# Kernel optimization log

Measured on AMD Instinct MI355X. Metric: run time of the kernel, lower is better.

Reference implementation:

```python
import jax, jax.numpy as jnp
import numpy as np
import math

NUM_BUCKETS = 32
MAX_DISTANCE = 128
N_HEADS = 16
D_KV = 64


def _relative_position_bucket(relative_position, num_buckets=NUM_BUCKETS, max_distance=MAX_DISTANCE):
    # bidirectional (encoder) variant
    num_buckets //= 2
    relative_buckets = (relative_position > 0).astype(jnp.int32) * num_buckets
    rp = jnp.abs(relative_position)
    max_exact = num_buckets // 2
    is_small = rp < max_exact
    rp_large = max_exact + (
        jnp.log(jnp.maximum(rp, 1).astype(jnp.float32) / max_exact)
        / math.log(max_distance / max_exact)
        * (num_buckets - max_exact)
    ).astype(jnp.int32)
    rp_large = jnp.minimum(rp_large, num_buckets - 1)
    return relative_buckets + jnp.where(is_small, rp, rp_large)


def compute_bias(rel_bias, q_len, k_len):
    ctx = jnp.arange(q_len)[:, None]
    mem = jnp.arange(k_len)[None, :]
    buckets = _relative_position_bucket(mem - ctx)          # [q, k]
    values = rel_bias[buckets]                               # [q, k, h]
    return jnp.transpose(values, (2, 0, 1))[None]            # [1, h, q, k]


def setup_inputs() -> dict:
    key = jax.random.key(0)
    ks = jax.random.split(key, 6)
    d_model, inner = 1024, N_HEADS * D_KV
    s = 0.02
    return {
        "hidden_states": jax.random.normal(ks[0], (2, 2048, d_model), jnp.float32),
        "Wq": jax.random.normal(ks[1], (d_model, inner), jnp.float32) * s,
        "Wk": jax.random.normal(ks[2], (d_model, inner), jnp.float32) * s,
        "Wv": jax.random.normal(ks[3], (d_model, inner), jnp.float32) * s,
        "Wo": jax.random.normal(ks[4], (inner, d_model), jnp.float32) * s,
        "rel_bias": jax.random.normal(ks[5], (NUM_BUCKETS, N_HEADS), jnp.float32) * s,
    }


def reference(hidden_states, Wq, Wk, Wv, Wo, rel_bias):
    B, S, D = hidden_states.shape

    def split_heads(x):  # [B,S,inner] -> [B,H,S,dk]
        return x.reshape(B, S, N_HEADS, D_KV).transpose(0, 2, 1, 3)

    q = split_heads(hidden_states @ Wq)
    k = split_heads(hidden_states @ Wk)
    v = split_heads(hidden_states @ Wv)

    # T5 does NOT scale by 1/sqrt(d_kv)
    scores = jnp.einsum("bhqd,bhkd->bhqk", q, k)
    scores = scores + compute_bias(rel_bias, S, S)
    attn = jax.nn.softmax(scores, axis=-1)
    ctx = jnp.einsum("bhqk,bhkd->bhqd", attn, v)
    ctx = ctx.transpose(0, 2, 1, 3).reshape(B, S, N_HEADS * D_KV)
    return ctx @ Wo
```

## Files before the change

### kernel.cpp

```cpp
#include <hip/hip_runtime.h>
#include <hip/hip_bf16.h>

typedef __bf16 bf16x8 __attribute__((ext_vector_type(8)));
typedef __bf16 bf16x4 __attribute__((ext_vector_type(4)));
typedef float floatx4 __attribute__((ext_vector_type(4)));
using bf16 = __hip_bfloat16;

#define S_    2048
#define NHEAD 16
#define LOG2E 1.4426950408889634f

__device__ __forceinline__ void load_lds16(const bf16* g, void* lds) {
  __builtin_amdgcn_global_load_lds((const __attribute__((address_space(1))) void*)g,
                                   (__attribute__((address_space(3))) void*)lds, 16, 0, 0);
}

__global__ void prep_kernel(const float* __restrict__ hidden,
                            const float* __restrict__ wq, const float* __restrict__ wk,
                            const float* __restrict__ wv, const float* __restrict__ wo,
                            const float* __restrict__ rel_bias,
                            bf16* __restrict__ hbf, bf16* __restrict__ wt_qkv,
                            bf16* __restrict__ wt_o, float* __restrict__ tab) {
  __shared__ bf16 tile[32][33];
  int bid = blockIdx.x;
  if (bid < 4096) {
    int i = (bid * 256 + threadIdx.x) * 4;
    float4 v = *(const float4*)(hidden + i);
    bf16 o[4] = {__float2bfloat16(v.x), __float2bfloat16(v.y),
                 __float2bfloat16(v.z), __float2bfloat16(v.w)};
    *(uint2*)(hbf + i) = *(const uint2*)o;
  } else if (bid < 8192) {
    int r = bid - 4096;
    int mat = r >> 10;
    int rem = r & 1023;
    int n0 = (rem & 31) * 32, k0 = (rem >> 5) * 32;
    int tx = threadIdx.x & 31, ty = threadIdx.x >> 5;
    const float* src = (mat == 0) ? wq : (mat == 1) ? wk : (mat == 2) ? wv : wo;
    bf16* dst = (mat == 3) ? wt_o : wt_qkv + mat * 1024 * 1024;
#pragma unroll
    for (int j = 0; j < 32; j += 8)
      tile[ty + j][tx] = __float2bfloat16(src[(k0 + ty + j) * 1024 + n0 + tx]);
    __syncthreads();
#pragma unroll
    for (int j = 0; j < 32; j += 8)
      dst[(n0 + ty + j) * 1024 + k0 + tx] = tile[tx][ty + j];
  } else {
    int idx = (bid - 8192) * 256 + threadIdx.x;
    int h = idx >> 12, j = idx & 4095;
    int delta = j - 2048;
    int rb = (delta > 0) ? 16 : 0;
    int rpa = delta < 0 ? -delta : delta;
    int bsmall;
    if (rpa < 8) {
      bsmall = rpa;
    } else {
      int lg = 25 - __clz(rpa * rpa);
      bsmall = 8 + lg;
      if (bsmall > 15) bsmall = 15;
    }
    tab[idx] = rel_bias[(rb + bsmall) * 16 + h] * LOG2E;
  }
}

__global__ __launch_bounds__(256) void gemm_qkv_kernel(const bf16* __restrict__ A,
                                                       const bf16* __restrict__ Bt,
                                                       bf16* __restrict__ qh,
                                                       bf16* __restrict__ kf,
                                                       bf16* __restrict__ vf) {
  const int K = 1024;
  __shared__ bf16 As[128 * 32];
  __shared__ bf16 Bs[128 * 32];
  int t = threadIdx.x;
  int m0 = blockIdx.y * 128, n0 = blockIdx.x * 128;
  int w = t >> 6, lane = t & 63, ln = lane & 15, quad = lane >> 4;
  int wr = w >> 1, wc = w & 1;
  floatx4 acc[4][4];
  floatx4 zero = {0.f, 0.f, 0.f, 0.f};
#pragma unroll
  for (int i = 0; i < 4; i++)
#pragma unroll
    for (int j = 0; j < 4; j++) acc[i][j] = zero;

  int r = t >> 2, c = (t & 3) * 8;
  const bf16* Ag = A + (long)(m0 + r) * K + c;
  const bf16* Bg = Bt + (long)(n0 + r) * K + c;
  char* ldsA0 = (char*)As + w * 1024;
  char* ldsA1 = ldsA0 + 4096;
  char* ldsB0 = (char*)Bs + w * 1024;
  char* ldsB1 = ldsB0 + 4096;

  for (int k0 = 0; k0 < K; k0 += 32) {
    load_lds16(Ag + k0, ldsA0);
    load_lds16(Ag + (long)64 * K + k0, ldsA1);
    load_lds16(Bg + k0, ldsB0);
    load_lds16(Bg + (long)64 * K + k0, ldsB1);
    __syncthreads();
    bf16x8 af[4], bfv[4];
#pragma unroll
    for (int i = 0; i < 4; i++)
      af[i] = *(const bf16x8*)&As[(wr * 64 + i * 16 + ln) * 32 + quad * 8];
#pragma unroll
    for (int j = 0; j < 4; j++)
      bfv[j] = *(const bf16x8*)&Bs[(wc * 64 + j * 16 + ln) * 32 + quad * 8];
#pragma unroll
    for (int i = 0; i < 4; i++)
#pragma unroll
      for (int j = 0; j < 4; j++)
        acc[i][j] = __builtin_amdgcn_mfma_f32_16x16x32_bf16(af[i], bfv[j], acc[i][j], 0, 0, 0);
    __syncthreads();
  }

  int nb = n0 + wc * 64;
  int type = nb >> 10, h = (nb >> 6) & 15;
  int b = (m0 >> 11);
  int sl0 = (m0 & 2047) + wr * 64;
  long bhbase = (long)((b * 16 + h)) * 131072;

  if (type == 0) {
#pragma unroll
    for (int i = 0; i < 4; i++)
#pragma unroll
      for (int j = 0; j < 4; j++) {
        int d = j * 16 + ln;
#pragma unroll
        for (int rr = 0; rr < 4; rr++) {
          int s = sl0 + i * 16 + quad * 4 + rr;
          qh[bhbase + (long)s * 64 + d] = __float2bfloat16(acc[i][j][rr]);
        }
      }
  } else if (type == 1) {
#pragma unroll
    for (int i = 0; i < 4; i++)
#pragma unroll
      for (int j = 0; j < 4; j++) {
        int d = j * 16 + ln;
        int dpart = (d >> 5) * 512 + ((d >> 3) & 3) * 128 + (d & 7);
        int kb = (sl0 + i * 16) * 64;
#pragma unroll
        for (int rr = 0; rr < 4; rr++)
          kf[bhbase + kb + dpart + (quad * 4 + rr) * 8] = __float2bfloat16(acc[i][j][rr]);
      }
  } else {
#pragma unroll
    for (int i = 0; i < 4; i++)
#pragma unroll
      for (int j = 0; j < 4; j++) {
        int off = (sl0 + (i >> 1) * 32) * 64 + j * 512 +
                  ((quad >> 1) + ((i & 1) << 1)) * 128 + ln * 8 + (quad & 1) * 4;
        bf16x4 pk = {(__bf16)acc[i][j][0], (__bf16)acc[i][j][1],
                     (__bf16)acc[i][j][2], (__bf16)acc[i][j][3]};
        *(bf16x4*)(vf + bhbase + off) = pk;
      }
  }
}

__global__ __launch_bounds__(256, 2) void attn_kernel(const bf16* __restrict__ qh,
                                                      const bf16* __restrict__ kf,
                                                      const bf16* __restrict__ vf,
                                                      const float* __restrict__ btab,
                                                      bf16* __restrict__ ctx) {
  __shared__ char PsRaw[4 * 2048];
  __shared__ char KV[2][16384];
  int t = threadIdx.x, w = t >> 6, lane = t & 63, ln = lane & 15, quad = lane >> 4;
  int bh = blockIdx.x, b = bh >> 4, h = bh & 15;
  int qw = blockIdx.y * 64 + w * 16;

  const bf16* qbase = qh + (long)bh * S_ * 64;
  const bf16* kfb = kf + (long)bh * S_ * 64;
  const bf16* vfb = vf + (long)bh * S_ * 64;
  const float* bt = btab + h * 4096;
  char* myPs = PsRaw + w * 2048;
  int lbo = quad * 256 + ln * 16;

  bf16x8 Qf0, Qf1;
  {
    const bf16* qr = qbase + (long)(qw + ln) * 64;
    Qf0 = *(const bf16x8*)(qr + quad * 8);
    Qf1 = *(const bf16x8*)(qr + 32 + quad * 8);
  }

  float cneg = bt[0], cpos = bt[4095];
  float l_acc = 0.f;
  floatx4 o[4];
  floatx4 zero = {0.f, 0.f, 0.f, 0.f};
#pragma unroll
  for (int dt = 0; dt < 4; dt++) o[dt] = zero;

  {
    const bf16* kg = kfb + t * 8;
    const bf16* vg = vfb + t * 8;
    load_lds16(kg,        KV[0] + w * 1024);
    load_lds16(kg + 2048, KV[0] + 4096 + w * 1024);
    load_lds16(vg,        KV[0] + 8192 + w * 1024);
    load_lds16(vg + 2048, KV[0] + 12288 + w * 1024);
  }

  int pb = 0;
  for (int k0 = 0; k0 < S_; k0 += 64) {
    __syncthreads();
    int kn = k0 + 64;
    if (kn < S_) {
      const bf16* kg = kfb + (long)kn * 64 + t * 8;
      const bf16* vg = vfb + (long)kn * 64 + t * 8;
      char* nb_ = KV[pb ^ 1];
      load_lds16(kg,        nb_ + w * 1024);
      load_lds16(kg + 2048, nb_ + 4096 + w * 1024);
      load_lds16(vg,        nb_ + 8192 + w * 1024);
      load_lds16(vg + 2048, nb_ + 12288 + w * 1024);
    }

    const char* bK = KV[pb];
    const char* bV = KV[pb] + 8192;
    bf16x8 Kr[4][2], Vr[4][2];
#pragma unroll
    for (int tile = 0; tile < 4; tile++) {
      Kr[tile][0] = *(const bf16x8*)(bK + tile * 2048 + lbo);
      Kr[tile][1] = *(const bf16x8*)(bK + tile * 2048 + 1024 + lbo);
    }
#pragma unroll
    for (int f = 0; f < 2; f++)
#pragma unroll
      for (int dt = 0; dt < 4; dt++)
        Vr[dt][f] = *(const bf16x8*)(bV + f * 4096 + dt * 1024 + lbo);

    bool near = (k0 > qw - 192) && (k0 < qw + 144);
    float bl[16];
    if (near) {
      int bb = k0 + quad * 4 - (qw + ln) + 2048;
#pragma unroll
      for (int tile = 0; tile < 4; tile++)
#pragma unroll
        for (int rr = 0; rr < 4; rr++)
          bl[tile * 4 + rr] = bt[bb + tile * 16 + rr];
    }

    floatx4 st[4];
#pragma unroll
    for (int tile = 0; tile < 4; tile++) {
      st[tile] = __builtin_amdgcn_mfma_f32_16x16x32_bf16(Kr[tile][0], Qf0, zero, 0, 0, 0);
      st[tile] = __builtin_amdgcn_mfma_f32_16x16x32_bf16(Kr[tile][1], Qf1, st[tile], 0, 0, 0);
    }

    if (near) {
#pragma unroll
      for (int tile = 0; tile < 4; tile++) {
        float p0 = __builtin_amdgcn_exp2f(fmaf(st[tile][0], LOG2E, bl[tile * 4 + 0]));
        float p1 = __builtin_amdgcn_exp2f(fmaf(st[tile][1], LOG2E, bl[tile * 4 + 1]));
        float p2 = __builtin_amdgcn_exp2f(fmaf(st[tile][2], LOG2E, bl[tile * 4 + 2]));
        float p3 = __builtin_amdgcn_exp2f(fmaf(st[tile][3], LOG2E, bl[tile * 4 + 3]));
        l_acc += (p0 + p1) + (p2 + p3);
        bf16x4 pk = {(__bf16)p0, (__bf16)p1, (__bf16)p2, (__bf16)p3};
        int chunk = tile * 2 + (quad >> 1);
        *(bf16x4*)(myPs + (ln * 8 + (chunk ^ (ln & 7))) * 16 + (quad & 1) * 8) = pk;
      }
    } else {
      float cb = (k0 > qw) ? cpos : cneg;
#pragma unroll
      for (int tile = 0; tile < 4; tile++) {
        float p0 = __builtin_amdgcn_exp2f(fmaf(st[tile][0], LOG2E, cb));
        float p1 = __builtin_amdgcn_exp2f(fmaf(st[tile][1], LOG2E, cb));
        float p2 = __builtin_amdgcn_exp2f(fmaf(st[tile][2], LOG2E, cb));
        float p3 = __builtin_amdgcn_exp2f(fmaf(st[tile][3], LOG2E, cb));
        l_acc += (p0 + p1) + (p2 + p3);
        bf16x4 pk = {(__bf16)p0, (__bf16)p1, (__bf16)p2, (__bf16)p3};
        int chunk = tile * 2 + (quad >> 1);
        *(bf16x4*)(myPs + (ln * 8 + (chunk ^ (ln & 7))) * 16 + (quad & 1) * 8) = pk;
      }
    }

    bf16x8 Pf0 = *(const bf16x8*)(myPs + (ln * 8 + (quad ^ (ln & 7))) * 16);
    bf16x8 Pf1 = *(const bf16x8*)(myPs + (ln * 8 + ((4 + quad) ^ (ln & 7))) * 16);
#pragma unroll
    for (int dt = 0; dt < 4; dt++) {
      o[dt] = __builtin_amdgcn_mfma_f32_16x16x32_bf16(Pf0, Vr[dt][0], o[dt], 0, 0, 0);
      o[dt] = __builtin_amdgcn_mfma_f32_16x16x32_bf16(Pf1, Vr[dt][1], o[dt], 0, 0, 0);
    }

    pb ^= 1;
  }

  l_acc += __shfl_xor(l_acc, 16);
  l_acc += __shfl_xor(l_acc, 32);
#pragma unroll
  for (int rr = 0; rr < 4; rr++) {
    float linv = 1.0f / __shfl(l_acc, quad * 4 + rr);
    int q = qw + quad * 4 + rr;
#pragma unroll
    for (int dt = 0; dt < 4; dt++)
      ctx[(long)(b * S_ + q) * 1024 + h * 64 + dt * 16 + ln] =
          __float2bfloat16(o[dt][rr] * linv);
  }
}

__global__ __launch_bounds__(256) void gemm_bt_kernel(const bf16* __restrict__ A,
                                                      const bf16* __restrict__ Bt,
                                                      float* __restrict__ C,
                                                      int M, int N, int K) {
  __shared__ bf16 As[128 * 32];
  __shared__ bf16 Bs[128 * 32];
  int t = threadIdx.x;
  int m0 = blockIdx.y * 128, n0 = blockIdx.x * 128;
  int w = t >> 6, lane = t & 63, ln = lane & 15, quad = lane >> 4;
  int wr = w >> 1, wc = w & 1;
  floatx4 acc[4][4];
  floatx4 zero = {0.f, 0.f, 0.f, 0.f};
#pragma unroll
  for (int i = 0; i < 4; i++)
#pragma unroll
    for (int j = 0; j < 4; j++) acc[i][j] = zero;

  int r = t >> 2, c = (t & 3) * 8;
  const bf16* Ag = A + (long)(m0 + r) * K + c;
  const bf16* Bg = Bt + (long)(n0 + r) * K + c;
  char* ldsA0 = (char*)As + w * 1024;
  char* ldsA1 = ldsA0 + 4096;
  char* ldsB0 = (char*)Bs + w * 1024;
  char* ldsB1 = ldsB0 + 4096;

  for (int k0 = 0; k0 < K; k0 += 32) {
    load_lds16(Ag + k0, ldsA0);
    load_lds16(Ag + (long)64 * K + k0, ldsA1);
    load_lds16(Bg + k0, ldsB0);
    load_lds16(Bg + (long)64 * K + k0, ldsB1);
    __syncthreads();
    bf16x8 af[4], bfv[4];
#pragma unroll
    for (int i = 0; i < 4; i++)
      af[i] = *(const bf16x8*)&As[(wr * 64 + i * 16 + ln) * 32 + quad * 8];
#pragma unroll
    for (int j = 0; j < 4; j++)
      bfv[j] = *(const bf16x8*)&Bs[(wc * 64 + j * 16 + ln) * 32 + quad * 8];
#pragma unroll
    for (int i = 0; i < 4; i++)
#pragma unroll
      for (int j = 0; j < 4; j++)
        acc[i][j] = __builtin_amdgcn_mfma_f32_16x16x32_bf16(af[i], bfv[j], acc[i][j], 0, 0, 0);
    __syncthreads();
  }

#pragma unroll
  for (int i = 0; i < 4; i++)
#pragma unroll
    for (int j = 0; j < 4; j++)
#pragma unroll
      for (int rr = 0; rr < 4; rr++)
        C[(long)(m0 + wr * 64 + i * 16 + quad * 4 + rr) * N + n0 + wc * 64 + j * 16 + ln] =
            acc[i][j][rr];
}

extern "C" void kernel_launch(void* const* d_in, const int* in_sizes, int n_in,
                              void* d_out, int out_size, void* d_ws, size_t ws_size,
                              hipStream_t stream) {
  (void)in_sizes; (void)n_in; (void)out_size; (void)ws_size;
  const float* hidden   = (const float*)d_in[0];
  const float* Wq       = (const float*)d_in[1];
  const float* Wk       = (const float*)d_in[2];
  const float* Wv       = (const float*)d_in[3];
  const float* Wo       = (const float*)d_in[4];
  const float* rel_bias = (const float*)d_in[5];

  char* ws = (char*)d_ws;
  bf16*  hbf    = (bf16*)(ws + 0);
  bf16*  wt_qkv = (bf16*)(ws + 8388608);
  bf16*  wt_o   = (bf16*)(ws + 14680064);
  float* btab   = (float*)(ws + 16777216);
  bf16*  qh     = (bf16*)(ws + 17039360);
  bf16*  kf     = (bf16*)(ws + 25427968);
  bf16*  vf     = (bf16*)(ws + 33816576);
  bf16*  ctx    = (bf16*)(ws + 42205184);

  prep_kernel<<<dim3(8448), dim3(256), 0, stream>>>(hidden, Wq, Wk, Wv, Wo, rel_bias,
                                                    hbf, wt_qkv, wt_o, btab);
  gemm_qkv_kernel<<<dim3(24, 32), dim3(256), 0, stream>>>(hbf, wt_qkv, qh, kf, vf);
  attn_kernel<<<dim3(32, 32), dim3(256), 0, stream>>>(qh, kf, vf, btab, ctx);
  gemm_bt_kernel<<<dim3(8, 32), dim3(256), 0, stream>>>(ctx, wt_o, (float*)d_out, 4096, 1024, 1024);
}
```

Baseline: 200.8 us.

## Process two query tiles per wave in attention to reuse K/V fragments

The attention kernel now runs 2 waves per block instead of 4, with each wave handling 32 query rows (two 16-row tiles). K and V fragments loaded from LDS are reused across both query tiles, which halves LDS reads per query and halves the number of waves issuing global-to-LDS loads. The cost is roughly twice the accumulator and score registers per wave and fewer waves per block, so occupancy and latency hiding may drop. Bias table values are now read directly inside the exp loop instead of being preloaded.

New measurement: 200.7 us. About the same (-0.0%).

```diff
diff --git a/kernel.cpp b/kernel.cpp
--- a/kernel.cpp
+++ b/kernel.cpp
@@ -154,45 +154,49 @@
   }
 }
 
-__global__ __launch_bounds__(256, 2) void attn_kernel(const bf16* __restrict__ qh,
+__global__ __launch_bounds__(128, 2) void attn_kernel(const bf16* __restrict__ qh,
                                                       const bf16* __restrict__ kf,
                                                       const bf16* __restrict__ vf,
                                                       const float* __restrict__ btab,
                                                       bf16* __restrict__ ctx) {
-  __shared__ char PsRaw[4 * 2048];
+  __shared__ char PsRaw[2 * 4096];
   __shared__ char KV[2][16384];
   int t = threadIdx.x, w = t >> 6, lane = t & 63, ln = lane & 15, quad = lane >> 4;
   int bh = blockIdx.x, b = bh >> 4, h = bh & 15;
-  int qw = blockIdx.y * 64 + w * 16;
+  int qw = blockIdx.y * 64 + w * 32;
 
   const bf16* qbase = qh + (long)bh * S_ * 64;
   const bf16* kfb = kf + (long)bh * S_ * 64;
   const bf16* vfb = vf + (long)bh * S_ * 64;
   const float* bt = btab + h * 4096;
-  char* myPs = PsRaw + w * 2048;
+  char* myPs = PsRaw + w * 4096;
   int lbo = quad * 256 + ln * 16;
 
-  bf16x8 Qf0, Qf1;
-  {
-    const bf16* qr = qbase + (long)(qw + ln) * 64;
-    Qf0 = *(const bf16x8*)(qr + quad * 8);
-    Qf1 = *(const bf16x8*)(qr + 32 + quad * 8);
+  bf16x8 Qf[2][2];
+#pragma unroll
+  for (int qt = 0; qt < 2; qt++) {
+    const bf16* qr = qbase + (long)(qw + qt * 16 + ln) * 64;
+    Qf[qt][0] = *(const bf16x8*)(qr + quad * 8);
+    Qf[qt][1] = *(const bf16x8*)(qr + 32 + quad * 8);
   }
 
   float cneg = bt[0], cpos = bt[4095];
-  float l_acc = 0.f;
-  floatx4 o[4];
+  float l_acc[2] = {0.f, 0.f};
+  floatx4 o[2][4];
   floatx4 zero = {0.f, 0.f, 0.f, 0.f};
 #pragma unroll
-  for (int dt = 0; dt < 4; dt++) o[dt] = zero;
+  for (int qt = 0; qt < 2; qt++)
+#pragma unroll
+    for (int dt = 0; dt < 4; dt++) o[qt][dt] = zero;
 
   {
     const bf16* kg = kfb + t * 8;
     const bf16* vg = vfb + t * 8;
-    load_lds16(kg,        KV[0] + w * 1024);
-    load_lds16(kg + 2048, KV[0] + 4096 + w * 1024);
-    load_lds16(vg,        KV[0] + 8192 + w * 1024);
-    load_lds16(vg + 2048, KV[0] + 12288 + w * 1024);
+#pragma unroll
+    for (int c = 0; c < 4; c++) {
+      load_lds16(kg + c * 1024, KV[0] + c * 2048 + w * 1024);
+      load_lds16(vg + c * 1024, KV[0] + 8192 + c * 2048 + w * 1024);
+    }
   }
 
   int pb = 0;
@@ -203,10 +207,11 @@
       const bf16* kg = kfb + (long)kn * 64 + t * 8;
       const bf16* vg = vfb + (long)kn * 64 + t * 8;
       char* nb_ = KV[pb ^ 1];
-      load_lds16(kg,        nb_ + w * 1024);
-      load_lds16(kg + 2048, nb_ + 4096 + w * 1024);
-      load_lds16(vg,        nb_ + 8192 + w * 1024);
-      load_lds16(vg + 2048, nb_ + 12288 + w * 1024);
+#pragma unroll
+      for (int c = 0; c < 4; c++) {
+        load_lds16(kg + c * 1024, nb_ + c * 2048 + w * 1024);
+        load_lds16(vg + c * 1024, nb_ + 8192 + c * 2048 + w * 1024);
+      }
     }
 
     const char* bK = KV[pb];
@@ -223,72 +228,78 @@
       for (int dt = 0; dt < 4; dt++)
         Vr[dt][f] = *(const bf16x8*)(bV + f * 4096 + dt * 1024 + lbo);
 
-    bool near = (k0 > qw - 192) && (k0 < qw + 144);
-    float bl[16];
-    if (near) {
-      int bb = k0 + quad * 4 - (qw + ln) + 2048;
-#pragma unroll
-      for (int tile = 0; tile < 4; tile++)
-#pragma unroll
-        for (int rr = 0; rr < 4; rr++)
-          bl[tile * 4 + rr] = bt[bb + tile * 16 + rr];
-    }
-
-    floatx4 st[4];
-#pragma unroll
-    for (int tile = 0; tile < 4; tile++) {
-      st[tile] = __builtin_amdgcn_mfma_f32_16x16x32_bf16(Kr[tile][0], Qf0, zero, 0, 0, 0);
-      st[tile] = __builtin_amdgcn_mfma_f32_16x16x32_bf16(Kr[tile][1], Qf1, st[tile], 0, 0, 0);
-    }
-
-    if (near) {
+    floatx4 st[2][4];
+#pragma unroll
+    for (int qt = 0; qt < 2; qt++)
 #pragma unroll
       for (int tile = 0; tile < 4; tile++) {
-        float p0 = __builtin_amdgcn_exp2f(fmaf(st[tile][0], LOG2E, bl[tile * 4 + 0]));
-        float p1 = __builtin_amdgcn_exp2f(fmaf(st[tile][1], LOG2E, bl[tile * 4 + 1]));
-        float p2 = __builtin_amdgcn_exp2f(fmaf(st[tile][2], LOG2E, bl[tile * 4 + 2]));
-        float p3 = __builtin_amdgcn_exp2f(fmaf(st[tile][3], LOG2E, bl[tile * 4 + 3]));
-        l_acc += (p0 + p1) + (p2 + p3);
-        bf16x4 pk = {(__bf16)p0, (__bf16)p1, (__bf16)p2, (__bf16)p3};
-        int chunk = tile * 2 + (quad >> 1);
-        *(bf16x4*)(myPs + (ln * 8 + (chunk ^ (ln & 7))) * 16 + (quad & 1) * 8) = pk;
-      }
-    } else {
-      float cb = (k0 > qw) ? cpos : cneg;
-#pragma unroll
-      for (int tile = 0; tile < 4; tile++) {
-        float p0 = __builtin_amdgcn_exp2f(fmaf(st[tile][0], LOG2E, cb));
-        float p1 = __builtin_amdgcn_exp2f(fmaf(st[tile][1], LOG2E, cb));
-        float p2 = __builtin_amdgcn_exp2f(fmaf(st[tile][2], LOG2E, cb));
-        float p3 = __builtin_amdgcn_exp2f(fmaf(st[tile][3], LOG2E, cb));
-        l_acc += (p0 + p1) + (p2 + p3);
-        bf16x4 pk = {(__bf16)p0, (__bf16)p1, (__bf16)p2, (__bf16)p3};
-        int chunk = tile * 2 + (quad >> 1);
-        *(bf16x4*)(myPs + (ln * 8 + (chunk ^ (ln & 7))) * 16 + (quad & 1) * 8) = pk;
-      }
-    }
-
-    bf16x8 Pf0 = *(const bf16x8*)(myPs + (ln * 8 + (quad ^ (ln & 7))) * 16);
-    bf16x8 Pf1 = *(const bf16x8*)(myPs + (ln * 8 + ((4 + quad) ^ (ln & 7))) * 16);
-#pragma unroll
-    for (int dt = 0; dt < 4; dt++) {
-      o[dt] = __builtin_amdgcn_mfma_f32_16x16x32_bf16(Pf0, Vr[dt][0], o[dt], 0, 0, 0);
-      o[dt] = __builtin_amdgcn_mfma_f32_16x16x32_bf16(Pf1, Vr[dt][1], o[dt], 0, 0, 0);
+        st[qt][tile] = __builtin_amdgcn_mfma_f32_16x16x32_bf16(Kr[tile][0], Qf[qt][0], zero, 0, 0, 0);
+        st[qt][tile] = __builtin_amdgcn_mfma_f32_16x16x32_bf16(Kr[tile][1], Qf[qt][1], st[qt][tile], 0, 0, 0);
+      }
+
+#pragma unroll
+    for (int qt = 0; qt < 2; qt++) {
+      int qwt = qw + qt * 16;
+      char* Ps = myPs + qt * 2048;
+      bool near = (k0 > qwt - 192) && (k0 < qwt + 144);
+      if (near) {
+#pragma unroll
+        for (int tile = 0; tile < 4; tile++) {
+          int bidx = k0 + tile * 16 + quad * 4 - (qwt + ln) + 2048;
+          float p0 = __builtin_amdgcn_exp2f(fmaf(st[qt][tile][0], LOG2E, bt[bidx + 0]));
+          float p1 = __builtin_amdgcn_exp2f(fmaf(st[qt][tile][1], LOG2E, bt[bidx + 1]));
+          float p2 = __builtin_amdgcn_exp2f(fmaf(st[qt][tile][2], LOG2E, bt[bidx + 2]));
+          float p3 = __builtin_amdgcn_exp2f(fmaf(st[qt][tile][3], LOG2E, bt[bidx + 3]));
+          l_acc[qt] += (p0 + p1) + (p2 + p3);
+          bf16x4 pk = {(__bf16)p0, (__bf16)p1, (__bf16)p2, (__bf16)p3};
+          int chunk = tile * 2 + (quad >> 1);
+          *(bf16x4*)(Ps + (ln * 8 + (chunk ^ (ln & 7))) * 16 + (quad & 1) * 8) = pk;
+        }
+      } else {
+        float cb = (k0 > qwt) ? cpos : cneg;
+#pragma unroll
+        for (int tile = 0; tile < 4; tile++) {
+          float p0 = __builtin_amdgcn_exp2f(fmaf(st[qt][tile][0], LOG2E, cb));
+          float p1 = __builtin_amdgcn_exp2f(fmaf(st[qt][tile][1], LOG2E, cb));
+          float p2 = __builtin_amdgcn_exp2f(fmaf(st[qt][tile][2], LOG2E, cb));
+          float p3 = __builtin_amdgcn_exp2f(fmaf(st[qt][tile][3], LOG2E, cb));
+          l_acc[qt] += (p0 + p1) + (p2 + p3);
+          bf16x4 pk = {(__bf16)p0, (__bf16)p1, (__bf16)p2, (__bf16)p3};
+          int chunk = tile * 2 + (quad >> 1);
+          *(bf16x4*)(Ps + (ln * 8 + (chunk ^ (ln & 7))) * 16 + (quad & 1) * 8) = pk;
+        }
+      }
+    }
+
+#pragma unroll
+    for (int qt = 0; qt < 2; qt++) {
+      char* Ps = myPs + qt * 2048;
+      bf16x8 Pf0 = *(const bf16x8*)(Ps + (ln * 8 + (quad ^ (ln & 7))) * 16);
+      bf16x8 Pf1 = *(const bf16x8*)(Ps + (ln * 8 + ((4 + quad) ^ (ln & 7))) * 16);
+#pragma unroll
+      for (int dt = 0; dt < 4; dt++) {
+        o[qt][dt] = __builtin_amdgcn_mfma_f32_16x16x32_bf16(Pf0, Vr[dt][0], o[qt][dt], 0, 0, 0);
+        o[qt][dt] = __builtin_amdgcn_mfma_f32_16x16x32_bf16(Pf1, Vr[dt][1], o[qt][dt], 0, 0, 0);
+      }
     }
 
     pb ^= 1;
   }
 
-  l_acc += __shfl_xor(l_acc, 16);
-  l_acc += __shfl_xor(l_acc, 32);
-#pragma unroll
-  for (int rr = 0; rr < 4; rr++) {
-    float linv = 1.0f / __shfl(l_acc, quad * 4 + rr);
-    int q = qw + quad * 4 + rr;
-#pragma unroll
-    for (int dt = 0; dt < 4; dt++)
-      ctx[(long)(b * S_ + q) * 1024 + h * 64 + dt * 16 + ln] =
-          __float2bfloat16(o[dt][rr] * linv);
+#pragma unroll
+  for (int qt = 0; qt < 2; qt++) {
+    float la = l_acc[qt];
+    la += __shfl_xor(la, 16);
+    la += __shfl_xor(la, 32);
+#pragma unroll
+    for (int rr = 0; rr < 4; rr++) {
+      float linv = 1.0f / __shfl(la, quad * 4 + rr);
+      int q = qw + qt * 16 + quad * 4 + rr;
+#pragma unroll
+      for (int dt = 0; dt < 4; dt++)
+        ctx[(long)(b * S_ + q) * 1024 + h * 64 + dt * 16 + ln] =
+            __float2bfloat16(o[qt][dt][rr] * linv);
+    }
   }
 }
 
@@ -372,6 +383,6 @@
   prep_kernel<<<dim3(8448), dim3(256), 0, stream>>>(hidden, Wq, Wk, Wv, Wo, rel_bias,
                                                     hbf, wt_qkv, wt_o, btab);
   gemm_qkv_kernel<<<dim3(24, 32), dim3(256), 0, stream>>>(hbf, wt_qkv, qh, kf, vf);
-  attn_kernel<<<dim3(32, 32), dim3(256), 0, stream>>>(qh, kf, vf, btab, ctx);
+  attn_kernel<<<dim3(32, 32), dim3(128), 0, stream>>>(qh, kf, vf, btab, ctx);
   gemm_bt_kernel<<<dim3(8, 32), dim3(256), 0, stream>>>(ctx, wt_o, (float*)d_out, 4096, 1024, 1024);
 }
```
